# Optimization experiments

Measured on AMD Instinct MI355X. Metric: run time of the kernel, lower is better.

Reference implementation:

```python
import jax, jax.numpy as jnp
import numpy as np

D_MODEL = 1024
NUM_HEADS = 16
HEAD_DIM = D_MODEL // NUM_HEADS
B, L = 2, 2048


def setup_inputs() -> dict:
    key = jax.random.key(0)
    ks = jax.random.split(key, 9)
    s = 0.02
    return {
        "query": jax.random.normal(ks[0], (B, L, D_MODEL), dtype=jnp.float32),
        "key": jax.random.normal(ks[1], (B, L, D_MODEL), dtype=jnp.float32),
        "value": jax.random.normal(ks[2], (B, L, D_MODEL), dtype=jnp.float32),
        "mask": jax.random.randint(ks[3], (B, L), 0, 2, dtype=jnp.int32),
        "Wq": jax.random.normal(ks[4], (D_MODEL, D_MODEL), dtype=jnp.float32) * s,
        "Wk": jax.random.normal(ks[5], (D_MODEL, D_MODEL), dtype=jnp.float32) * s,
        "Wv": jax.random.normal(ks[6], (D_MODEL, D_MODEL), dtype=jnp.float32) * s,
        "Wo": jax.random.normal(ks[7], (D_MODEL, D_MODEL), dtype=jnp.float32) * s,
        "bo": jnp.zeros((D_MODEL,), dtype=jnp.float32),
    }


def _split_heads(x):
    # (B, L, d_model) -> (B, H, L, head_dim)
    b, l, _ = x.shape
    return x.reshape(b, l, NUM_HEADS, HEAD_DIM).transpose(0, 2, 1, 3)


def reference(query, key, value, mask, Wq, Wk, Wv, Wo, bo):
    # nn.Linear(bias=False): x @ W.T
    q = _split_heads(query @ Wq.T)   # (B, H, L, hd)
    k = _split_heads(key @ Wk.T)
    v = _split_heads(value @ Wv.T)

    scores = jnp.einsum("bhqd,bhkd->bhqk", q, k) / jnp.sqrt(jnp.float32(HEAD_DIM))
    # padding mask over keys: (B, L) -> (B, 1, 1, L); 0 = pad -> -inf
    keep = (mask[:, None, None, :] != 0)
    scores = jnp.where(keep, scores, -jnp.inf)

    attn = jax.nn.softmax(scores, axis=-1)
    # original zeroes NaN rows (fully-masked query rows)
    attn = jnp.where(jnp.isnan(attn), jnp.zeros_like(attn), attn)
    # dropout is identity in eval/reference mode

    ctx = jnp.einsum("bhqk,bhkd->bhqd", attn, v)           # (B, H, L, hd)
    ctx = ctx.transpose(0, 2, 1, 3).reshape(B, L, D_MODEL)  # combine heads
    return ctx @ Wo.T + bo
```

## Files before the change

kernel.cpp:

```cpp
#include <hip/hip_runtime.h>

typedef unsigned short u16;
typedef __bf16 bf16x8 __attribute__((ext_vector_type(8)));
typedef __bf16 bf16x4 __attribute__((ext_vector_type(4)));
typedef float floatx4 __attribute__((ext_vector_type(4)));
typedef u16 u16x4 __attribute__((ext_vector_type(4)));

#define MEG ((size_t)(1u << 20))

__device__ __forceinline__ u16 f2bf(float f) {
  unsigned int u = __float_as_uint(f);
  u += 0x7fffu + ((u >> 16) & 1u);
  return (u16)(u >> 16);
}

__device__ __forceinline__ void load_lds16(const u16* g, u16* l) {
  __builtin_amdgcn_global_load_lds((const __attribute__((address_space(1))) unsigned int*)g,
                                   (__attribute__((address_space(3))) unsigned int*)l,
                                   16, 0, 0);
}

__global__ __launch_bounds__(256) void cvt7(
    const float* __restrict__ s0, const float* __restrict__ s1,
    const float* __restrict__ s2, const float* __restrict__ s3,
    const float* __restrict__ s4, const float* __restrict__ s5,
    const float* __restrict__ s6, u16* __restrict__ dst)
{
  size_t e = ((size_t)blockIdx.x * 256 + threadIdx.x) * 4;
  unsigned m = (unsigned)(e >> 20);
  const float* s; size_t off;
  if (m < 4)       { s = s0; off = e; }
  else if (m < 8)  { s = s1; off = e - 4 * MEG; }
  else if (m < 12) { s = s2; off = e - 8 * MEG; }
  else if (m < 13) { s = s3; off = e - 12 * MEG; }
  else if (m < 14) { s = s4; off = e - 13 * MEG; }
  else if (m < 15) { s = s5; off = e - 14 * MEG; }
  else             { s = s6; off = e - 15 * MEG; }
  float4 f = *reinterpret_cast<const float4*>(s + off);
  u16x4 o;
  o.x = f2bf(f.x); o.y = f2bf(f.y); o.z = f2bf(f.z); o.w = f2bf(f.w);
  *reinterpret_cast<u16x4*>(dst + e) = o;
}

template<int IT, bool OUT_BF16, bool ADD_BIAS, bool VT>
__global__ __launch_bounds__(256) void gemm_bt(
    const u16* __restrict__ Abase, const u16* __restrict__ Bbase,
    const float* __restrict__ bias, void* __restrict__ Cbase,
    u16* __restrict__ VtB,
    int M, int N, int K, long zA, long zB, long zC)
{
  __shared__ __align__(16) u16 As[IT * 32 * 64];
  __shared__ __align__(16) u16 Bs[128 * 64];
  const int tid = threadIdx.x;
  const int w = tid >> 6, ln = tid & 63;
  const int lm = ln & 15, lq = ln >> 4;
  const int wm = w >> 1, wn = w & 1;
  const long m0 = (long)blockIdx.y * (IT * 32), n0 = (long)blockIdx.x * 128;
  const u16* A = Abase + (size_t)blockIdx.z * (size_t)zA;
  const u16* B = Bbase + (size_t)blockIdx.z * (size_t)zB;

  const int r0 = tid >> 3;
  const int kc = (tid & 7) ^ (r0 & 7);
  const u16* gA = A + (m0 + r0) * (long)K + kc * 8;
  const u16* gB = B + (n0 + r0) * (long)K + kc * 8;
  const long rstep = 32L * K;

  const int sl0 = (lq ^ (lm & 7)) * 8;
  const int sl1 = ((4 + lq) ^ (lm & 7)) * 8;
  const u16* ab0 = &As[(wm * (IT * 16) + lm) * 64 + sl0];
  const u16* ab1 = &As[(wm * (IT * 16) + lm) * 64 + sl1];
  const u16* bb0 = &Bs[(wn * 64 + lm) * 64 + sl0];
  const u16* bb1 = &Bs[(wn * 64 + lm) * 64 + sl1];

  const floatx4 z4 = {0.f, 0.f, 0.f, 0.f};
  floatx4 acc[IT][4];
#pragma unroll
  for (int i = 0; i < IT; ++i)
#pragma unroll
    for (int j = 0; j < 4; ++j) acc[i][j] = z4;

  for (int k0 = 0; k0 < K; k0 += 64) {
#pragma unroll
    for (int t = 0; t < IT; ++t)
      load_lds16(gA + t * rstep, &As[(t * 256 + w * 64) * 8]);
#pragma unroll
    for (int t = 0; t < 4; ++t)
      load_lds16(gB + t * rstep, &Bs[(t * 256 + w * 64) * 8]);
    gA += 64; gB += 64;
    __syncthreads();
    bf16x8 af[IT][2], bfr[4][2];
#pragma unroll
    for (int i = 0; i < IT; ++i) {
      af[i][0] = *reinterpret_cast<const bf16x8*>(ab0 + i * 1024);
      af[i][1] = *reinterpret_cast<const bf16x8*>(ab1 + i * 1024);
    }
#pragma unroll
    for (int j = 0; j < 4; ++j) {
      bfr[j][0] = *reinterpret_cast<const bf16x8*>(bb0 + j * 1024);
      bfr[j][1] = *reinterpret_cast<const bf16x8*>(bb1 + j * 1024);
    }
#pragma unroll
    for (int i = 0; i < IT; ++i)
#pragma unroll
      for (int j = 0; j < 4; ++j) {
        acc[i][j] = __builtin_amdgcn_mfma_f32_16x16x32_bf16(af[i][0], bfr[j][0], acc[i][j], 0, 0, 0);
        acc[i][j] = __builtin_amdgcn_mfma_f32_16x16x32_bf16(af[i][1], bfr[j][1], acc[i][j], 0, 0, 0);
      }
    __syncthreads();
  }

  if (VT && blockIdx.z == 2) {
#pragma unroll
    for (int i = 0; i < IT; ++i) {
      long row = m0 + wm * (IT * 16) + i * 16 + lq * 4;
      int bq = (int)(row >> 11);
      int l  = (int)(row & 2047);
#pragma unroll
      for (int j = 0; j < 4; ++j) {
        long col = n0 + wn * 64 + j * 16 + lm;
        int hh = (int)(col >> 6), dd = (int)(col & 63);
        u16x4 o;
        o.x = f2bf(acc[i][j][0]); o.y = f2bf(acc[i][j][1]);
        o.z = f2bf(acc[i][j][2]); o.w = f2bf(acc[i][j][3]);
        *reinterpret_cast<u16x4*>(&VtB[((size_t)(bq * 16 + hh)) * 131072 +
                                       (size_t)dd * 2048 + l]) = o;
      }
    }
    return;
  }

#pragma unroll
  for (int i = 0; i < IT; ++i) {
    long row = m0 + wm * (IT * 16) + i * 16 + lq * 4;
#pragma unroll
    for (int j = 0; j < 4; ++j) {
      long col = n0 + wn * 64 + j * 16 + lm;
#pragma unroll
      for (int r = 0; r < 4; ++r) {
        float v = acc[i][j][r];
        if (ADD_BIAS) v += bias[col];
        size_t idx = (size_t)(row + r) * (size_t)N + (size_t)col;
        if (OUT_BF16) (((u16*)Cbase) + (size_t)blockIdx.z * (size_t)zC)[idx] = f2bf(v);
        else ((float*)Cbase)[idx] = v;
      }
    }
  }
}

__global__ __launch_bounds__(256, 4) void attn_kernel(
    const u16* __restrict__ Qp, const u16* __restrict__ Kp,
    const u16* __restrict__ Vt, const int* __restrict__ mask,
    u16* __restrict__ OpBase, float* __restrict__ psAB)
{
  __shared__ __align__(16) u16 Ks[64 * 64];
  __shared__ __align__(16) u16 Vts[64 * 64];
  __shared__ __align__(16) u16 Ps[4 * 32 * 64];
  __shared__ __align__(16) u16 mball[1024];

  const int tid = threadIdx.x;
  const int w = tid >> 6, ln = tid & 63;
  const int lm = ln & 15, lq = ln >> 4;
  const int bh = blockIdx.y, b = bh >> 4, h = bh & 15;
  const int q0 = blockIdx.x * 128;
  const int kz = blockIdx.z;

  const u16* Qh = Qp + (size_t)b * 2048 * 1024 + h * 64;
  const u16* Kh = Kp + (size_t)b * 2048 * 1024 + (size_t)kz * 1024 * 1024 + h * 64;
  const u16* Vth = Vt + (size_t)bh * 64 * 2048 + kz * 1024;
  u16* Op = OpBase + (size_t)kz * 8 * MEG;
  float* psZ = psAB + (size_t)kz * 65536;

  const int* mrowp = mask + b * 2048 + kz * 1024;
#pragma unroll
  for (int t = 0; t < 4; ++t) {
    int i = t * 256 + tid;
    mball[i] = (mrowp[i] != 0) ? (u16)0 : (u16)0xFF80;
  }

  bf16x8 qf[2][2];
#pragma unroll
  for (int m = 0; m < 2; ++m) {
    int qrow = q0 + w * 32 + m * 16 + lm;
    qf[m][0] = *reinterpret_cast<const bf16x8*>(Qh + (size_t)qrow * 1024 + lq * 8);
    qf[m][1] = *reinterpret_cast<const bf16x8*>(Qh + (size_t)qrow * 1024 + 32 + lq * 8);
  }

  const int sl0 = (lq ^ (lm & 7)) * 8;
  const int sl1 = ((4 + lq) ^ (lm & 7)) * 8;
  const u16* kb0 = &Ks[lm * 64 + sl0];
  const u16* kb1 = &Ks[lm * 64 + sl1];
  const u16* vb0 = &Vts[lm * 64 + sl0];
  const u16* vb1 = &Vts[lm * 64 + sl1];
  u16* Pw = &Ps[w * 2048];
  u16* pwr[4];
#pragma unroll
  for (int n = 0; n < 4; ++n) pwr[n] = &Pw[lm * 64 + (((4 * n + lq) ^ lm) * 4)];
  const u16* prd[4];
#pragma unroll
  for (int t = 0; t < 4; ++t)
    prd[t] = &Pw[lm * 64 + (((8 * (t >> 1) + 2 * lq + (t & 1)) ^ lm) * 4)];
  const u16* mbi = mball + lq * 4;

  const int r0 = tid >> 3;
  const int kc = (tid & 7) ^ (r0 & 7);
  const u16* gK0 = Kh + (size_t)r0 * 1024 + kc * 8;
  const u16* gK1 = gK0 + 32 * 1024;
  const u16* gV0 = Vth + (size_t)r0 * 2048 + kc * 8;
  const u16* gV1 = gV0 + 32 * 2048;

  const floatx4 z4 = {0.f, 0.f, 0.f, 0.f};
  floatx4 O[2][4];
#pragma unroll
  for (int m = 0; m < 2; ++m)
#pragma unroll
    for (int j = 0; j < 4; ++j) O[m][j] = z4;
  float psum[2] = {0.f, 0.f};
  const float SCL = 0.18033688011112042f;

  for (int it = 0; it < 16; ++it) {
    load_lds16(gK0, &Ks[(w * 64) * 8]);
    load_lds16(gK1, &Ks[(256 + w * 64) * 8]);
    load_lds16(gV0, &Vts[(w * 64) * 8]);
    load_lds16(gV1, &Vts[(256 + w * 64) * 8]);
    gK0 += 64 * 1024; gK1 += 64 * 1024; gV0 += 64; gV1 += 64;
    __syncthreads();

    bf16x8 kf[4][2], vf[4][2];
#pragma unroll
    for (int n = 0; n < 4; ++n) {
      kf[n][0] = *reinterpret_cast<const bf16x8*>(kb0 + n * 1024);
      kf[n][1] = *reinterpret_cast<const bf16x8*>(kb1 + n * 1024);
    }
#pragma unroll
    for (int j = 0; j < 4; ++j) {
      vf[j][0] = *reinterpret_cast<const bf16x8*>(vb0 + j * 1024);
      vf[j][1] = *reinterpret_cast<const bf16x8*>(vb1 + j * 1024);
    }
    float mb4[4][4];
#pragma unroll
    for (int n = 0; n < 4; ++n) {
      u16x4 mv = *reinterpret_cast<const u16x4*>(mbi + n * 16);
      mb4[n][0] = __uint_as_float((unsigned)mv.x << 16);
      mb4[n][1] = __uint_as_float((unsigned)mv.y << 16);
      mb4[n][2] = __uint_as_float((unsigned)mv.z << 16);
      mb4[n][3] = __uint_as_float((unsigned)mv.w << 16);
    }
    mbi += 64;

#pragma unroll
    for (int m = 0; m < 2; ++m) {
      floatx4 S[4];
#pragma unroll
      for (int n = 0; n < 4; ++n) {
        S[n] = __builtin_amdgcn_mfma_f32_16x16x32_bf16(kf[n][0], qf[m][0], z4, 0, 0, 0);
        S[n] = __builtin_amdgcn_mfma_f32_16x16x32_bf16(kf[n][1], qf[m][1], S[n], 0, 0, 0);
      }

#pragma unroll
      for (int n = 0; n < 4; ++n) {
        float p0 = __builtin_amdgcn_exp2f(fmaf(S[n][0], SCL, mb4[n][0]));
        float p1 = __builtin_amdgcn_exp2f(fmaf(S[n][1], SCL, mb4[n][1]));
        float p2 = __builtin_amdgcn_exp2f(fmaf(S[n][2], SCL, mb4[n][2]));
        float p3 = __builtin_amdgcn_exp2f(fmaf(S[n][3], SCL, mb4[n][3]));
        psum[m] += (p0 + p1) + (p2 + p3);
        unsigned u0 = __float_as_uint(p0) + 0x8000u;
        unsigned u1 = __float_as_uint(p1) + 0x8000u;
        unsigned u2 = __float_as_uint(p2) + 0x8000u;
        unsigned u3 = __float_as_uint(p3) + 0x8000u;
        uint2 pk;
        pk.x = __builtin_amdgcn_perm(u1, u0, 0x07060302u);
        pk.y = __builtin_amdgcn_perm(u3, u2, 0x07060302u);
        *reinterpret_cast<uint2*>(pwr[n] + m * 1024) = pk;
      }

#pragma unroll
      for (int h2 = 0; h2 < 2; ++h2) {
        bf16x4 pa = *reinterpret_cast<const bf16x4*>(prd[2 * h2] + m * 1024);
        bf16x4 pb = *reinterpret_cast<const bf16x4*>(prd[2 * h2 + 1] + m * 1024);
        bf16x8 pf = __builtin_shufflevector(pa, pb, 0, 1, 2, 3, 4, 5, 6, 7);
#pragma unroll
        for (int j = 0; j < 4; ++j)
          O[m][j] = __builtin_amdgcn_mfma_f32_16x16x32_bf16(pf, vf[j][h2], O[m][j], 0, 0, 0);
      }
    }
    __syncthreads();
  }

#pragma unroll
  for (int m = 0; m < 2; ++m) {
    float s = psum[m];
    s += __shfl_xor(s, 16, 64);
    s += __shfl_xor(s, 32, 64);
    int prow = q0 + w * 32 + m * 16 + lm;
    if (lq == 0) psZ[bh * 2048 + prow] = s;
#pragma unroll
    for (int r = 0; r < 4; ++r) {
      int row = q0 + w * 32 + m * 16 + lq * 4 + r;
      size_t base = ((size_t)b * 2048 + row) * 1024 + h * 64 + lm;
#pragma unroll
      for (int j = 0; j < 4; ++j)
        Op[base + j * 16] = f2bf(O[m][j][r]);
    }
  }
}

__global__ __launch_bounds__(256) void combine_norm(
    const u16* __restrict__ Oa, const u16* __restrict__ Ob,
    const float* __restrict__ psA, const float* __restrict__ psB,
    u16* __restrict__ ctx)
{
  size_t idx = ((size_t)blockIdx.x * 256 + threadIdx.x) * 8;
  int q = (int)(idx >> 10);
  int c = (int)(idx & 1023);
  int b = q >> 11, l = q & 2047, h = c >> 6;
  int ql = (b * 16 + h) * 2048 + l;
  float s = psA[ql] + psB[ql];
  float inv = (s > 0.f) ? 1.0f / s : 0.f;

  uint4 ua = *reinterpret_cast<const uint4*>(Oa + idx);
  uint4 ub = *reinterpret_cast<const uint4*>(Ob + idx);
  uint4 uo;
  const unsigned* pa = reinterpret_cast<const unsigned*>(&ua);
  const unsigned* pb = reinterpret_cast<const unsigned*>(&ub);
  unsigned* po = reinterpret_cast<unsigned*>(&uo);
#pragma unroll
  for (int i = 0; i < 4; ++i) {
    float alo = __uint_as_float(pa[i] << 16);
    float ahi = __uint_as_float(pa[i] & 0xFFFF0000u);
    float blo = __uint_as_float(pb[i] << 16);
    float bhi = __uint_as_float(pb[i] & 0xFFFF0000u);
    float olo = (alo + blo) * inv;
    float ohi = (ahi + bhi) * inv;
    po[i] = (unsigned)f2bf(olo) | ((unsigned)f2bf(ohi) << 16);
  }
  *reinterpret_cast<uint4*>(ctx + idx) = uo;
}

extern "C" void kernel_launch(void* const* d_in, const int* in_sizes, int n_in,
                              void* d_out, int out_size, void* d_ws, size_t ws_size,
                              hipStream_t stream) {
  const float* q  = (const float*)d_in[0];
  const float* k  = (const float*)d_in[1];
  const float* v  = (const float*)d_in[2];
  const int*   mk = (const int*)  d_in[3];
  const float* wq = (const float*)d_in[4];
  const float* wk = (const float*)d_in[5];
  const float* wv = (const float*)d_in[6];
  const float* wo = (const float*)d_in[7];
  const float* bo = (const float*)d_in[8];

  u16* ws16 = (u16*)d_ws;
  u16* Xq  = ws16;
  u16* Wq  = ws16 + 12 * MEG;
  u16* Wo  = ws16 + 15 * MEG;
  u16* Qp  = ws16 + 16 * MEG;
  u16* Kp  = ws16 + 20 * MEG;
  u16* Vt  = ws16 + 24 * MEG;
  u16* OpA = ws16;
  u16* OpB = ws16 + 8 * MEG;
  float* psAB = (float*)(ws16 + 12 * MEG);
  u16* ctx = ws16 + 4 * MEG;

  cvt7<<<dim3(16384), dim3(256), 0, stream>>>(q, k, v, wq, wk, wv, wo, ws16);

  gemm_bt<4, true, false, true><<<dim3(8, 32, 3), dim3(256), 0, stream>>>(
      Xq, Wq, nullptr, (void*)Qp, Vt, 4096, 1024, 1024,
      (long)(4 * MEG), (long)MEG, (long)(4 * MEG));

  attn_kernel<<<dim3(16, 32, 2), dim3(256), 0, stream>>>(Qp, Kp, Vt, mk, OpA, psAB);

  combine_norm<<<dim3(2048), dim3(256), 0, stream>>>(OpA, OpB, psAB, psAB + 65536, ctx);

  gemm_bt<2, false, true, false><<<dim3(8, 64, 1), dim3(256), 0, stream>>>(
      ctx, Wo, bo, d_out, nullptr, 4096, 1024, 1024, 0, 0, 0);
}
```

Measured before the change: 222.6 us.

## Double-buffer K/V tiles in attention kernel to overlap loads with compute

Adds a second LDS buffer for K and V tiles and prefetches the next tile with global_load_lds while the current tile is being computed. Explicit waitcnt plus barrier replace the load-then-sync pattern, so the memory wait should be hidden behind MFMA work. To keep LDS use in check, the per-wave P scratch is halved and reused across the two m sub-tiles, and launch bounds drop from 4 to 3 blocks per CU. Risks are lower occupancy, a hazard on reusing the P buffer between m iterations within a wave, and fragile hand-encoded waitcnt values.

Result: slower. 232.1 us (+4.3%).

```diff
diff --git a/kernel.cpp b/kernel.cpp
--- a/kernel.cpp
+++ b/kernel.cpp
@@ -147,14 +147,14 @@
   }
 }
 
-__global__ __launch_bounds__(256, 4) void attn_kernel(
+__global__ __launch_bounds__(256, 3) void attn_kernel(
     const u16* __restrict__ Qp, const u16* __restrict__ Kp,
     const u16* __restrict__ Vt, const int* __restrict__ mask,
     u16* __restrict__ OpBase, float* __restrict__ psAB)
 {
-  __shared__ __align__(16) u16 Ks[64 * 64];
-  __shared__ __align__(16) u16 Vts[64 * 64];
-  __shared__ __align__(16) u16 Ps[4 * 32 * 64];
+  __shared__ __align__(16) u16 Ks[2][64 * 64];
+  __shared__ __align__(16) u16 Vts[2][64 * 64];
+  __shared__ __align__(16) u16 Ps[4 * 16 * 64];
   __shared__ __align__(16) u16 mball[1024];
 
   const int tid = threadIdx.x;
@@ -187,11 +187,8 @@
 
   const int sl0 = (lq ^ (lm & 7)) * 8;
   const int sl1 = ((4 + lq) ^ (lm & 7)) * 8;
-  const u16* kb0 = &Ks[lm * 64 + sl0];
-  const u16* kb1 = &Ks[lm * 64 + sl1];
-  const u16* vb0 = &Vts[lm * 64 + sl0];
-  const u16* vb1 = &Vts[lm * 64 + sl1];
-  u16* Pw = &Ps[w * 2048];
+  const int kof0 = lm * 64 + sl0, kof1 = lm * 64 + sl1;
+  u16* Pw = &Ps[w * 1024];
   u16* pwr[4];
 #pragma unroll
   for (int n = 0; n < 4; ++n) pwr[n] = &Pw[lm * 64 + (((4 * n + lq) ^ lm) * 4)];
@@ -217,25 +214,31 @@
   float psum[2] = {0.f, 0.f};
   const float SCL = 0.18033688011112042f;
 
+  load_lds16(gK0, &Ks[0][w * 512]);
+  load_lds16(gK1, &Ks[0][2048 + w * 512]);
+  load_lds16(gV0, &Vts[0][w * 512]);
+  load_lds16(gV1, &Vts[0][2048 + w * 512]);
+  gK0 += 64 * 1024; gK1 += 64 * 1024; gV0 += 64; gV1 += 64;
+  __syncthreads();
+
   for (int it = 0; it < 16; ++it) {
-    load_lds16(gK0, &Ks[(w * 64) * 8]);
-    load_lds16(gK1, &Ks[(256 + w * 64) * 8]);
-    load_lds16(gV0, &Vts[(w * 64) * 8]);
-    load_lds16(gV1, &Vts[(256 + w * 64) * 8]);
-    gK0 += 64 * 1024; gK1 += 64 * 1024; gV0 += 64; gV1 += 64;
-    __syncthreads();
-
-    bf16x8 kf[4][2], vf[4][2];
-#pragma unroll
-    for (int n = 0; n < 4; ++n) {
-      kf[n][0] = *reinterpret_cast<const bf16x8*>(kb0 + n * 1024);
-      kf[n][1] = *reinterpret_cast<const bf16x8*>(kb1 + n * 1024);
-    }
-#pragma unroll
-    for (int j = 0; j < 4; ++j) {
-      vf[j][0] = *reinterpret_cast<const bf16x8*>(vb0 + j * 1024);
-      vf[j][1] = *reinterpret_cast<const bf16x8*>(vb1 + j * 1024);
-    }
+    const int cur = it & 1;
+    if (it < 15) {
+      const int nxt = cur ^ 1;
+      load_lds16(gK0, &Ks[nxt][w * 512]);
+      load_lds16(gK1, &Ks[nxt][2048 + w * 512]);
+      load_lds16(gV0, &Vts[nxt][w * 512]);
+      load_lds16(gV1, &Vts[nxt][2048 + w * 512]);
+      gK0 += 64 * 1024; gK1 += 64 * 1024; gV0 += 64; gV1 += 64;
+      __builtin_amdgcn_s_waitcnt(0x0F74);
+    } else {
+      __builtin_amdgcn_s_waitcnt(0x0F70);
+    }
+    __builtin_amdgcn_s_barrier();
+
+    const u16* kb = &Ks[cur][0];
+    const u16* vb = &Vts[cur][0];
+
     float mb4[4][4];
 #pragma unroll
     for (int n = 0; n < 4; ++n) {
@@ -246,6 +249,18 @@
       mb4[n][3] = __uint_as_float((unsigned)mv.w << 16);
     }
     mbi += 64;
+
+    bf16x8 kf[4][2], vf[4][2];
+#pragma unroll
+    for (int n = 0; n < 4; ++n) {
+      kf[n][0] = *reinterpret_cast<const bf16x8*>(kb + n * 1024 + kof0);
+      kf[n][1] = *reinterpret_cast<const bf16x8*>(kb + n * 1024 + kof1);
+    }
+#pragma unroll
+    for (int j = 0; j < 4; ++j) {
+      vf[j][0] = *reinterpret_cast<const bf16x8*>(vb + j * 1024 + kof0);
+      vf[j][1] = *reinterpret_cast<const bf16x8*>(vb + j * 1024 + kof1);
+    }
 
 #pragma unroll
     for (int m = 0; m < 2; ++m) {
@@ -270,20 +285,20 @@
         uint2 pk;
         pk.x = __builtin_amdgcn_perm(u1, u0, 0x07060302u);
         pk.y = __builtin_amdgcn_perm(u3, u2, 0x07060302u);
-        *reinterpret_cast<uint2*>(pwr[n] + m * 1024) = pk;
+        *reinterpret_cast<uint2*>(pwr[n]) = pk;
       }
 
 #pragma unroll
       for (int h2 = 0; h2 < 2; ++h2) {
-        bf16x4 pa = *reinterpret_cast<const bf16x4*>(prd[2 * h2] + m * 1024);
-        bf16x4 pb = *reinterpret_cast<const bf16x4*>(prd[2 * h2 + 1] + m * 1024);
+        bf16x4 pa = *reinterpret_cast<const bf16x4*>(prd[2 * h2]);
+        bf16x4 pb = *reinterpret_cast<const bf16x4*>(prd[2 * h2 + 1]);
         bf16x8 pf = __builtin_shufflevector(pa, pb, 0, 1, 2, 3, 4, 5, 6, 7);
 #pragma unroll
         for (int j = 0; j < 4; ++j)
           O[m][j] = __builtin_amdgcn_mfma_f32_16x16x32_bf16(pf, vf[j][h2], O[m][j], 0, 0, 0);
       }
     }
-    __syncthreads();
+    __builtin_amdgcn_s_barrier();
   }
 
 #pragma unroll
```
